# Kernel tuning notes

Hardware: AMD Instinct MI355X
Metric: run time of the kernel (lower is better)

## Reference

```python
import jax, jax.numpy as jnp
import numpy as np

B, P, ENC = 128, 196, 512
H = 512   # must equal ENC (gate * awe elementwise in original)
E = 512   # embed size
A = 512   # attention dim
V = 32000
L = 20    # caption length; decode steps T = L - 1


def setup_inputs() -> dict:
    key = jax.random.key(0)
    ks = jax.random.split(key, 24)
    s = 0.02
    features = jax.random.normal(ks[0], (B, P, ENC), jnp.float32)
    captions = jax.random.randint(ks[1], (B, L), 0, V)
    # lengths sorted descending (pack_padded_sequence contract); force max = L
    len_np = np.sort(np.array(jax.random.randint(ks[2], (B,), 2, L + 1)))[::-1].copy()
    len_np[0] = L
    lengths = jnp.asarray(len_np, jnp.int32)
    rn = lambda k, sh: jax.random.normal(k, sh, jnp.float32) * s
    return {
        "features": features, "captions": captions, "lengths": lengths,
        "w_enc_att": rn(ks[3], (A, ENC)), "b_enc_att": rn(ks[4], (A,)),
        "w_dec_att": rn(ks[5], (A, H)), "b_dec_att": rn(ks[6], (A,)),
        "w_full": rn(ks[7], (A,)), "b_full": rn(ks[8], (1,)),
        "embed_w": rn(ks[9], (V, E)),
        "w_ih": rn(ks[10], (4 * H, E + ENC)), "b_ih": rn(ks[11], (4 * H,)),
        "w_hh": rn(ks[12], (4 * H, H)), "b_hh": rn(ks[13], (4 * H,)),
        "w_init_h": rn(ks[14], (H, ENC)), "b_init_h": rn(ks[15], (H,)),
        "w_init_c": rn(ks[16], (H, ENC)), "b_init_c": rn(ks[17], (H,)),
        "w_beta": rn(ks[18], (H, ENC)), "b_beta": rn(ks[19], (H,)),
        "w_fc": rn(ks[20], (V, H)), "b_fc": rn(ks[21], (V,)),
    }


def _decode(features, captions, lengths, w_enc_att, b_enc_att, w_dec_att,
            b_dec_att, w_full, b_full, embed_w, w_ih, b_ih, w_hh, b_hh,
            w_init_h, b_init_h, w_init_c, b_init_c, w_beta, b_beta, w_fc, b_fc):
    T = captions.shape[1] - 1  # static max decode length
    dec_len = lengths - 1      # [B]
    emb = embed_w[captions]    # [B, L, E]
    fmean = features.mean(axis=1)                       # [B, ENC]
    h0 = fmean @ w_init_h.T + b_init_h                  # [B, H]
    c0 = fmean @ w_init_c.T + b_init_c
    att1 = features @ w_enc_att.T + b_enc_att           # [B, P, A] (precomputed, step-invariant)

    xs_emb = jnp.swapaxes(emb[:, :T, :], 0, 1)          # [T, B, E]
    active = jnp.arange(T)[:, None] < dec_len[None, :]  # [T, B], mimics batch_size_t slicing

    def step(carry, xs):
        h, c = carry
        x_t, act = xs                                   # [B,E], [B]
        m = act[:, None]
        # additive attention
        att2 = h @ w_dec_att.T + b_dec_att              # [B, A]
        e = jnp.einsum('bpa,a->bp', jax.nn.relu(att1 + att2[:, None, :]), w_full) + b_full[0]
        alpha = jax.nn.softmax(e, axis=1)               # [B, P]
        awe = jnp.einsum('bp,bpe->be', alpha, features) # [B, ENC]
        gate = jax.nn.sigmoid(h @ w_beta.T + b_beta)    # [B, H] (H == ENC)
        awe = gate * awe
        # LSTMCell (torch gate order i, f, g, o)
        z = jnp.concatenate([x_t, awe], axis=1)         # [B, E+ENC]
        gates = z @ w_ih.T + b_ih + h @ w_hh.T + b_hh   # [B, 4H]
        i_g, f_g, g_g, o_g = jnp.split(gates, 4, axis=1)
        c_new = jax.nn.sigmoid(f_g) * c + jax.nn.sigmoid(i_g) * jnp.tanh(g_g)
        h_new = jax.nn.sigmoid(o_g) * jnp.tanh(c_new)
        # inactive rows keep old state (torch only updates h[:batch_size_t])
        h2 = jnp.where(m, h_new, h)
        c2 = jnp.where(m, c_new, c)
        preds = h_new @ w_fc.T + b_fc                   # dropout in eval mode (identity)
        preds = jnp.where(m, preds, 0.0)
        alpha_o = jnp.where(m, alpha, 0.0)
        return (h2, c2), (preds, alpha_o)

    (_, _), (preds_t, alphas_t) = jax.lax.scan(step, (h0, c0), (xs_emb, active))
    predictions = jnp.swapaxes(preds_t, 0, 1)           # [B, T, V]
    alphas = jnp.swapaxes(alphas_t, 0, 1)               # [B, T, P]
    return predictions, alphas


def reference(features, captions, lengths, w_enc_att, b_enc_att, w_dec_att,
              b_dec_att, w_full, b_full, embed_w, w_ih, b_ih, w_hh, b_hh,
              w_init_h, b_init_h, w_init_c, b_init_c, w_beta, b_beta, w_fc, b_fc):
    return _decode(features, captions, lengths, w_enc_att, b_enc_att, w_dec_att,
                   b_dec_att, w_full, b_full, embed_w, w_ih, b_ih, w_hh, b_hh,
                   w_init_h, b_init_h, w_init_c, b_init_c, w_beta, b_beta,
                   w_fc, b_fc)
```

## Files before the change

kernel.cpp:

```cpp
#include <hip/hip_runtime.h>
#include <hip/hip_bf16.h>

typedef __attribute__((ext_vector_type(8))) short short8;
typedef __attribute__((ext_vector_type(4))) float floatx4;

#define NB 128
#define NP 196
#define NH 512
#define NV 32000
#define NT 19

__device__ __forceinline__ float bf2f(short s) {
  unsigned int u = ((unsigned int)(unsigned short)s) << 16;
  return __builtin_bit_cast(float, u);
}
__device__ __forceinline__ short f2bf(float f) {
  unsigned int u = __builtin_bit_cast(unsigned int, f);
  unsigned int lsb = (u >> 16) & 1u;
  u += 0x7fffu + lsb;
  return (short)(u >> 16);
}
__device__ __forceinline__ float sigf(float x) { return 1.f / (1.f + expf(-x)); }
__device__ __forceinline__ float ldw(int fl, const void* p, int i) {
  return fl ? bf2f(((const short*)p)[i]) : ((const float*)p)[i];
}

__global__ void k_detect(const unsigned int* __restrict__ w, int* __restrict__ flagp) {
  __shared__ int cnt;
  if (threadIdx.x == 0) cnt = 0;
  __syncthreads();
  int local = 0;
  for (int i = threadIdx.x; i < 4096; i += 256) {
    unsigned int lo = w[i] & 0xFFFFu;
    unsigned int ex = (lo >> 7) & 0xFFu;
    if (ex >= 110u && ex <= 135u) local++;
  }
  atomicAdd(&cnt, local);
  __syncthreads();
  if (threadIdx.x == 0) *flagp = (cnt > 2048) ? 1 : 0;
}

__global__ void k_convall(const void* __restrict__ s0, const void* __restrict__ s1,
                          const void* __restrict__ s2, const void* __restrict__ s3,
                          const void* __restrict__ s4, const void* __restrict__ s5,
                          const void* __restrict__ s6, const void* __restrict__ s7,
                          const void* __restrict__ s8, const void* __restrict__ s9,
                          short* __restrict__ dst, const int* __restrict__ flagp) {
  int fl = *flagp;
  const int totc = 50069504 / 8;
  for (int c = blockIdx.x * 256 + threadIdx.x; c < totc; c += gridDim.x * 256) {
    int i = c * 8;
    const void* src;
    int off;
    if (i < 12845056)      { src = s0; off = i; }
    else if (i < 29229056) { src = s1; off = i - 12845056; }
    else if (i < 45613056) { src = s2; off = i - 29229056; }
    else if (i < 47710208) { src = s3; off = i - 45613056; }
    else if (i < 48758784) { src = s4; off = i - 47710208; }
    else if (i < 49020928) { src = s5; off = i - 48758784; }
    else if (i < 49283072) { src = s6; off = i - 49020928; }
    else if (i < 49545216) { src = s7; off = i - 49283072; }
    else if (i < 49807360) { src = s8; off = i - 49545216; }
    else                   { src = s9; off = i - 49807360; }
    if (fl) {
      ((short8*)dst)[c] = *(const short8*)((const short*)src + off);
    } else {
      const float* sp = (const float*)src + off;
      short8 o;
#pragma unroll
      for (int j = 0; j < 8; ++j) o[j] = f2bf(sp[j]);
      ((short8*)dst)[c] = o;
    }
  }
}

__global__ void k_fmean(const short* __restrict__ feat, short* __restrict__ fmean) {
  int b = blockIdx.x;
  for (int e = threadIdx.x; e < NH; e += 256) {
    float s = 0.f;
    const short* fp = feat + (size_t)b * (NP * NH) + e;
    for (int p = 0; p < NP; ++p) s += bf2f(fp[p * NH]);
    fmean[b * NH + e] = f2bf(s * (1.f / 196.f));
  }
}

__global__ void k_init(const short* __restrict__ fmean,
                       const short* __restrict__ w_init_h, const void* __restrict__ b_init_h,
                       const short* __restrict__ w_init_c, const void* __restrict__ b_init_c,
                       short* __restrict__ hbuf, float* __restrict__ cbuf,
                       const int* __restrict__ flagp) {
  int fl = *flagp;
  int wave = threadIdx.x >> 6, lane = threadIdx.x & 63;
  int rlo = lane & 15, quad = lane >> 4;
  int n = (blockIdx.x * 4 + wave) * 16 + rlo;
  const short* brow = (n < 512 ? w_init_h + (size_t)n * 512 : w_init_c + (size_t)(n - 512) * 512) + quad * 8;
  const short* arow = fmean + rlo * 512 + quad * 8;
  floatx4 acc[8];
#pragma unroll
  for (int mt = 0; mt < 8; ++mt) acc[mt] = (floatx4){0.f, 0.f, 0.f, 0.f};
  for (int k = 0; k < 512; k += 32) {
    short8 bfr = *(const short8*)(brow + k);
#pragma unroll
    for (int mt = 0; mt < 8; ++mt) {
      short8 afr = *(const short8*)(arow + mt * (16 * 512) + k);
      acc[mt] = __builtin_amdgcn_mfma_f32_16x16x32_bf16(afr, bfr, acc[mt], 0, 0, 0);
    }
  }
  float bias = (n < 512) ? ldw(fl, b_init_h, n) : ldw(fl, b_init_c, n - 512);
#pragma unroll
  for (int mt = 0; mt < 8; ++mt)
#pragma unroll
    for (int r = 0; r < 4; ++r) {
      int bb = mt * 16 + quad * 4 + r;
      float v = acc[mt][r] + bias;
      if (n < 512) hbuf[bb * 512 + n] = f2bf(v);
      else cbuf[bb * 512 + (n - 512)] = v;
    }
}

__global__ void k_att1(const short* __restrict__ feat, const short* __restrict__ w_enc,
                       const void* __restrict__ b_enc, short* __restrict__ att1,
                       const int* __restrict__ flagp) {
  int fl = *flagp;
  int wave = threadIdx.x >> 6, lane = threadIdx.x & 63;
  int rlo = lane & 15, quad = lane >> 4;
  int n = (blockIdx.x * 4 + wave) * 16 + rlo;
  int mbase = blockIdx.y * 128;
  const short* brow = w_enc + (size_t)n * 512 + quad * 8;
  const short* arow = feat + (size_t)(mbase + rlo) * 512 + quad * 8;
  floatx4 acc[8];
#pragma unroll
  for (int mt = 0; mt < 8; ++mt) acc[mt] = (floatx4){0.f, 0.f, 0.f, 0.f};
  for (int k = 0; k < 512; k += 32) {
    short8 bfr = *(const short8*)(brow + k);
#pragma unroll
    for (int mt = 0; mt < 8; ++mt) {
      short8 afr = *(const short8*)(arow + (size_t)mt * (16 * 512) + k);
      acc[mt] = __builtin_amdgcn_mfma_f32_16x16x32_bf16(afr, bfr, acc[mt], 0, 0, 0);
    }
  }
  float bias = ldw(fl, b_enc, n);
#pragma unroll
  for (int mt = 0; mt < 8; ++mt)
#pragma unroll
    for (int r = 0; r < 4; ++r) {
      int m = mbase + mt * 16 + quad * 4 + r;
      att1[(size_t)m * 512 + n] = f2bf(acc[mt][r] + bias);
    }
}

__global__ void k_xpart(const int* __restrict__ captions, const short* __restrict__ embed_w,
                        const short* __restrict__ w_ih, const void* __restrict__ b_ih,
                        const void* __restrict__ b_hh, float* __restrict__ xp,
                        const int* __restrict__ flagp) {
  int fl = *flagp;
  int wave = threadIdx.x >> 6, lane = threadIdx.x & 63;
  int rlo = lane & 15, quad = lane >> 4;
  int t = blockIdx.y;
  int n = (blockIdx.x * 4 + wave) * 16 + rlo;
  const short* brow = w_ih + (size_t)n * 1024 + quad * 8;
  int tok[8];
#pragma unroll
  for (int mt = 0; mt < 8; ++mt) tok[mt] = captions[(mt * 16 + rlo) * 20 + t];
  floatx4 acc[8];
#pragma unroll
  for (int mt = 0; mt < 8; ++mt) acc[mt] = (floatx4){0.f, 0.f, 0.f, 0.f};
  for (int k = 0; k < 512; k += 32) {
    short8 bfr = *(const short8*)(brow + k);
#pragma unroll
    for (int mt = 0; mt < 8; ++mt) {
      short8 afr = *(const short8*)(embed_w + (size_t)tok[mt] * 512 + quad * 8 + k);
      acc[mt] = __builtin_amdgcn_mfma_f32_16x16x32_bf16(afr, bfr, acc[mt], 0, 0, 0);
    }
  }
  float bias = ldw(fl, b_ih, n) + ldw(fl, b_hh, n);
#pragma unroll
  for (int mt = 0; mt < 8; ++mt)
#pragma unroll
    for (int r = 0; r < 4; ++r) {
      int bb = mt * 16 + quad * 4 + r;
      xp[((size_t)t * 128 + bb) * 2048 + n] = acc[mt][r] + bias;
    }
}

__global__ void k_hproj(const short* __restrict__ hbuf,
                        const short* __restrict__ w_dec, const void* __restrict__ b_dec,
                        const short* __restrict__ w_beta, const void* __restrict__ b_beta,
                        const short* __restrict__ w_hh, float* __restrict__ abuf,
                        const int* __restrict__ flagp) {
  int fl = *flagp;
  int wave = threadIdx.x >> 6, lane = threadIdx.x & 63;
  int rlo = lane & 15, quad = lane >> 4;
  int n = (blockIdx.x * 4 + wave) * 16 + rlo;
  const short* brow;
  float bias;
  if (n < 512)       { brow = w_dec  + (size_t)n * 512;          bias = ldw(fl, b_dec, n); }
  else if (n < 1024) { brow = w_beta + (size_t)(n - 512) * 512;  bias = ldw(fl, b_beta, n - 512); }
  else               { brow = w_hh   + (size_t)(n - 1024) * 512; bias = 0.f; }
  brow += quad * 8;
  const short* arow = hbuf + rlo * 512 + quad * 8;
  floatx4 acc[8];
#pragma unroll
  for (int mt = 0; mt < 8; ++mt) acc[mt] = (floatx4){0.f, 0.f, 0.f, 0.f};
  for (int k = 0; k < 512; k += 32) {
    short8 bfr = *(const short8*)(brow + k);
#pragma unroll
    for (int mt = 0; mt < 8; ++mt) {
      short8 afr = *(const short8*)(arow + mt * (16 * 512) + k);
      acc[mt] = __builtin_amdgcn_mfma_f32_16x16x32_bf16(afr, bfr, acc[mt], 0, 0, 0);
    }
  }
#pragma unroll
  for (int mt = 0; mt < 8; ++mt)
#pragma unroll
    for (int r = 0; r < 4; ++r) {
      int bb = mt * 16 + quad * 4 + r;
      abuf[(size_t)bb * 3072 + n] = acc[mt][r] + bias;
    }
}

__global__ void k_score(const short* __restrict__ att1, const float* __restrict__ abuf,
                        const void* __restrict__ w_full, float* __restrict__ escore,
                        const int* __restrict__ flagp) {
  int fl = *flagp;
  int wave = threadIdx.x >> 6, lane = threadIdx.x & 63;
  int gw = blockIdx.x * 4 + wave;
  int r0 = gw * 8;
  float wfr[8];
#pragma unroll
  for (int j = 0; j < 8; ++j) wfr[j] = ldw(fl, w_full, lane * 8 + j);
#pragma unroll
  for (int rr = 0; rr < 8; ++rr) {
    int r = r0 + rr;
    int b = r / 196;
    const float* a2 = abuf + (size_t)b * 3072 + lane * 8;
    floatx4 a2a = *(const floatx4*)a2;
    floatx4 a2b = *(const floatx4*)(a2 + 4);
    short8 v = *(const short8*)(att1 + (size_t)r * 512 + lane * 8);
    float s = 0.f;
    s += fmaxf(bf2f(v[0]) + a2a[0], 0.f) * wfr[0];
    s += fmaxf(bf2f(v[1]) + a2a[1], 0.f) * wfr[1];
    s += fmaxf(bf2f(v[2]) + a2a[2], 0.f) * wfr[2];
    s += fmaxf(bf2f(v[3]) + a2a[3], 0.f) * wfr[3];
    s += fmaxf(bf2f(v[4]) + a2b[0], 0.f) * wfr[4];
    s += fmaxf(bf2f(v[5]) + a2b[1], 0.f) * wfr[5];
    s += fmaxf(bf2f(v[6]) + a2b[2], 0.f) * wfr[6];
    s += fmaxf(bf2f(v[7]) + a2b[3], 0.f) * wfr[7];
#pragma unroll
    for (int off = 32; off >= 1; off >>= 1) s += __shfl_xor(s, off, 64);
    if (lane == 0) escore[r] = s;
  }
}

__global__ void k_ctx(const float* __restrict__ escore, const short* __restrict__ feat,
                      const float* __restrict__ abuf, const int* __restrict__ lengths,
                      short* __restrict__ awe, void* __restrict__ d_out,
                      const int* __restrict__ flagp, int t) {
  int fl = *flagp;
  int ec = blockIdx.x;
  int b = blockIdx.y;
  int tid = threadIdx.x, wave = tid >> 6, lane = tid & 63;
  __shared__ float sm[196];
  __shared__ float psum[4][128];
  for (int p = tid; p < NP; p += 256) sm[p] = escore[b * NP + p];
  __syncthreads();
  bool act = t < (lengths[b] - 1);
  if (wave == 0) {
    float v0 = sm[lane], v1 = sm[lane + 64], v2 = sm[lane + 128];
    float v3 = (lane < 4) ? sm[lane + 192] : -1e30f;
    float m = fmaxf(fmaxf(v0, v1), fmaxf(v2, v3));
#pragma unroll
    for (int off = 32; off >= 1; off >>= 1) m = fmaxf(m, __shfl_xor(m, off, 64));
    float e0 = expf(v0 - m), e1 = expf(v1 - m), e2 = expf(v2 - m);
    float e3 = (lane < 4) ? expf(v3 - m) : 0.f;
    float s = e0 + e1 + e2 + e3;
#pragma unroll
    for (int off = 32; off >= 1; off >>= 1) s += __shfl_xor(s, off, 64);
    float inv = 1.f / s;
    float a0 = e0 * inv, a1 = e1 * inv, a2 = e2 * inv, a3 = e3 * inv;
    sm[lane] = a0; sm[lane + 64] = a1; sm[lane + 128] = a2;
    if (lane < 4) sm[lane + 192] = a3;
    if (ec == 0) {
      size_t ob = (size_t)NB * NT * NV + ((size_t)b * NT + t) * NP;
      float o0 = act ? a0 : 0.f, o1 = act ? a1 : 0.f, o2 = act ? a2 : 0.f, o3 = act ? a3 : 0.f;
      if (fl) {
        short* op = (short*)d_out;
        op[ob + lane] = f2bf(o0); op[ob + lane + 64] = f2bf(o1); op[ob + lane + 128] = f2bf(o2);
        if (lane < 4) op[ob + lane + 192] = f2bf(o3);
      } else {
        float* op = (float*)d_out;
        op[ob + lane] = o0; op[ob + lane + 64] = o1; op[ob + lane + 128] = o2;
        if (lane < 4) op[ob + lane + 192] = o3;
      }
    }
  }
  __syncthreads();
  int eoff = ec * 128 + lane * 2;
  const short* fb = feat + (size_t)b * (NP * NH) + eoff;
  float acc0 = 0.f, acc1 = 0.f;
  for (int p = wave; p < NP; p += 4) {
    unsigned int u = *(const unsigned int*)(fb + (size_t)p * NH);
    float al = sm[p];
    acc0 = fmaf(al, __builtin_bit_cast(float, u << 16), acc0);
    acc1 = fmaf(al, __builtin_bit_cast(float, u & 0xFFFF0000u), acc1);
  }
  psum[wave][lane * 2] = acc0;
  psum[wave][lane * 2 + 1] = acc1;
  __syncthreads();
  if (tid < 128) {
    int e = ec * 128 + tid;
    float s = psum[0][tid] + psum[1][tid] + psum[2][tid] + psum[3][tid];
    float gate = sigf(abuf[(size_t)b * 3072 + 512 + e]);
    awe[b * NH + e] = f2bf(gate * s);
  }
}

__global__ void k_gates_lstm(const short* __restrict__ awe_bf, const short* __restrict__ w_ih,
                             const float* __restrict__ xp, const float* __restrict__ abuf,
                             const int* __restrict__ lengths, float* __restrict__ cbuf,
                             short* __restrict__ hbuf, short* __restrict__ hnall, int t) {
  int tid = threadIdx.x, wave = tid >> 6, lane = tid & 63;
  int rlo = lane & 15, quad = lane >> 4;
  int n = wave * 512 + blockIdx.x * 16 + rlo;
  const short* brow = w_ih + (size_t)n * 1024 + 512 + quad * 8;
  const short* arow = awe_bf + rlo * 512 + quad * 8;
  floatx4 acc[8];
#pragma unroll
  for (int mt = 0; mt < 8; ++mt) acc[mt] = (floatx4){0.f, 0.f, 0.f, 0.f};
  for (int k = 0; k < 512; k += 32) {
    short8 bfr = *(const short8*)(brow + k);
#pragma unroll
    for (int mt = 0; mt < 8; ++mt) {
      short8 afr = *(const short8*)(arow + mt * (16 * 512) + k);
      acc[mt] = __builtin_amdgcn_mfma_f32_16x16x32_bf16(afr, bfr, acc[mt], 0, 0, 0);
    }
  }
  __shared__ float gsm[4][128][17];
#pragma unroll
  for (int mt = 0; mt < 8; ++mt)
#pragma unroll
    for (int r = 0; r < 4; ++r) {
      int bb = mt * 16 + quad * 4 + r;
      float v = acc[mt][r] + xp[((size_t)t * 128 + bb) * 2048 + n] + abuf[(size_t)bb * 3072 + 1024 + n];
      gsm[wave][bb][rlo] = v;
    }
  __syncthreads();
  for (int idx = tid; idx < 2048; idx += 256) {
    int bb = idx >> 4, jl = idx & 15;
    int j = blockIdx.x * 16 + jl;
    float ig = gsm[0][bb][jl], fg = gsm[1][bb][jl], gg = gsm[2][bb][jl], og = gsm[3][bb][jl];
    float co = cbuf[bb * 512 + j];
    float cn = sigf(fg) * co + sigf(ig) * tanhf(gg);
    float hn = sigf(og) * tanhf(cn);
    hnall[(size_t)t * (128 * 512) + bb * 512 + j] = f2bf(hn);
    if (t < lengths[bb] - 1) {
      cbuf[bb * 512 + j] = cn;
      hbuf[bb * 512 + j] = f2bf(hn);
    }
  }
}

__global__ void k_preds_all(const short* __restrict__ hnall, const short* __restrict__ w_fc,
                            const void* __restrict__ b_fc, const int* __restrict__ lengths,
                            void* __restrict__ d_out, const int* __restrict__ flagp) {
  int fl = *flagp;
  int tid = threadIdx.x, wave = tid >> 6, lane = tid & 63;
  int rlo = lane & 15, quad = lane >> 4;
  int n0 = blockIdx.x * 128;
  int mh = (wave >> 1) * 64;
  int nh = (wave & 1) * 64;
  __shared__ short Al[128 * 128];
  __shared__ short Bl[128 * 128];

  float bias[4];
#pragma unroll
  for (int nf = 0; nf < 4; ++nf) bias[nf] = ldw(fl, b_fc, n0 + nh + nf * 16 + rlo);

  for (int t = 0; t < NT; ++t) {
    floatx4 acc[4][4];
#pragma unroll
    for (int mt = 0; mt < 4; ++mt)
#pragma unroll
      for (int nf = 0; nf < 4; ++nf) acc[mt][nf] = (floatx4){0.f, 0.f, 0.f, 0.f};

    for (int kc = 0; kc < 4; ++kc) {
#pragma unroll
      for (int j = 0; j < 8; ++j) {
        int idx = j * 256 + tid;
        int row = idx >> 4, c8 = idx & 15;
        int sw = (c8 * 16) ^ ((row & 7) << 4);
        short8 va = *(const short8*)(hnall + ((size_t)t * 128 + row) * 512 + kc * 128 + c8 * 8);
        *(short8*)((char*)Al + row * 256 + sw) = va;
        short8 vb = *(const short8*)(w_fc + (size_t)(n0 + row) * 512 + kc * 128 + c8 * 8);
        *(short8*)((char*)Bl + row * 256 + sw) = vb;
      }
      __syncthreads();
#pragma unroll
      for (int kkl = 0; kkl < 4; ++kkl) {
        int kb = kkl * 64 + quad * 16;
        short8 afr[4], bfr[4];
#pragma unroll
        for (int mt = 0; mt < 4; ++mt) {
          int row = mh + mt * 16 + rlo;
          afr[mt] = *(const short8*)((const char*)Al + row * 256 + (kb ^ ((row & 7) << 4)));
        }
#pragma unroll
        for (int nf = 0; nf < 4; ++nf) {
          int row = nh + nf * 16 + rlo;
          bfr[nf] = *(const short8*)((const char*)Bl + row * 256 + (kb ^ ((row & 7) << 4)));
        }
#pragma unroll
        for (int mt = 0; mt < 4; ++mt)
#pragma unroll
          for (int nf = 0; nf < 4; ++nf)
            acc[mt][nf] = __builtin_amdgcn_mfma_f32_16x16x32_bf16(afr[mt], bfr[nf], acc[mt][nf], 0, 0, 0);
      }
      __syncthreads();
    }
#pragma unroll
    for (int mt = 0; mt < 4; ++mt)
#pragma unroll
      for (int r = 0; r < 4; ++r) {
        int bb = mh + mt * 16 + quad * 4 + r;
        bool act = t < lengths[bb] - 1;
#pragma unroll
        for (int nf = 0; nf < 4; ++nf) {
          int n = n0 + nh + nf * 16 + rlo;
          float v = act ? (acc[mt][nf][r] + bias[nf]) : 0.f;
          size_t oi = ((size_t)bb * NT + t) * NV + n;
          if (fl) ((short*)d_out)[oi] = f2bf(v);
          else ((float*)d_out)[oi] = v;
        }
      }
  }
}

extern "C" void kernel_launch(void* const* d_in, const int* in_sizes, int n_in,
                              void* d_out, int out_size, void* d_ws, size_t ws_size,
                              hipStream_t stream) {
  const void* features = d_in[0];
  const int* captions = (const int*)d_in[1];
  const int* lengths = (const int*)d_in[2];
  const void* w_enc_att = d_in[3];
  const void* b_enc_att = d_in[4];
  const void* w_dec_att = d_in[5];
  const void* b_dec_att = d_in[6];
  const void* w_full = d_in[7];
  const void* embed_w = d_in[9];
  const void* w_ih = d_in[10];
  const void* b_ih = d_in[11];
  const void* w_hh = d_in[12];
  const void* b_hh = d_in[13];
  const void* w_init_h = d_in[14];
  const void* b_init_h = d_in[15];
  const void* w_init_c = d_in[16];
  const void* b_init_c = d_in[17];
  const void* w_beta = d_in[18];
  const void* b_beta = d_in[19];
  const void* w_fc = d_in[20];
  const void* b_fc = d_in[21];

  char* ws = (char*)d_ws;
  int* flagp = (int*)ws; ws += 16;
  short* cfeat = (short*)ws; ws += (size_t)12845056 * 2;
  short* cembed = (short*)ws; ws += (size_t)16384000 * 2;
  short* cwfc = (short*)ws; ws += (size_t)16384000 * 2;
  short* cwih = (short*)ws; ws += (size_t)2097152 * 2;
  short* cwhh = (short*)ws; ws += (size_t)1048576 * 2;
  short* cwenc = (short*)ws; ws += (size_t)262144 * 2;
  short* cwdec = (short*)ws; ws += (size_t)262144 * 2;
  short* cwbeta = (short*)ws; ws += (size_t)262144 * 2;
  short* cwinith = (short*)ws; ws += (size_t)262144 * 2;
  short* cwinitc = (short*)ws; ws += (size_t)262144 * 2;
  short* att1 = (short*)ws; ws += (size_t)25088 * 512 * 2;
  float* xp   = (float*)ws; ws += (size_t)2432 * 2048 * 4;
  float* abuf = (float*)ws; ws += (size_t)128 * 3072 * 4;
  float* escore = (float*)ws; ws += (size_t)25088 * 4;
  short* hbuf = (short*)ws; ws += 128 * 512 * 2;
  short* hnall = (short*)ws; ws += (size_t)NT * 128 * 512 * 2;
  short* awe  = (short*)ws; ws += 128 * 512 * 2;
  short* fmean = (short*)ws; ws += 128 * 512 * 2;
  float* cbuf = (float*)ws; ws += 128 * 512 * 4;

  k_detect<<<1, 256, 0, stream>>>((const unsigned int*)features, flagp);
  k_convall<<<2048, 256, 0, stream>>>(features, embed_w, w_fc, w_ih, w_hh,
                                      w_enc_att, w_dec_att, w_beta, w_init_h, w_init_c,
                                      cfeat, flagp);

  k_fmean<<<128, 256, 0, stream>>>(cfeat, fmean);
  k_att1<<<dim3(8, 196), 256, 0, stream>>>(cfeat, cwenc, b_enc_att, att1, flagp);
  k_xpart<<<dim3(32, NT), 256, 0, stream>>>(captions, cembed, cwih, b_ih, b_hh, xp, flagp);
  k_init<<<16, 256, 0, stream>>>(fmean, cwinith, b_init_h, cwinitc, b_init_c, hbuf, cbuf, flagp);

  for (int t = 0; t < NT; ++t) {
    k_hproj<<<48, 256, 0, stream>>>(hbuf, cwdec, b_dec_att, cwbeta, b_beta, cwhh, abuf, flagp);
    k_score<<<784, 256, 0, stream>>>(att1, abuf, w_full, escore, flagp);
    k_ctx<<<dim3(4, 128), 256, 0, stream>>>(escore, cfeat, abuf, lengths, awe, d_out, flagp, t);
    k_gates_lstm<<<32, 256, 0, stream>>>(awe, cwih, xp, abuf, lengths, cbuf, hbuf, hnall, t);
  }
  k_preds_all<<<250, 256, 0, stream>>>(hnall, cwfc, b_fc, lengths, d_out, flagp);
}
```

Baseline: 2.689 ms.

## Keep w_fc tile resident in LDS across timesteps in output projection

The vocab projection kernel now loads a 64-row slice of w_fc (full K=512) into shared memory once and reuses it for all 19 timesteps. Activations are read straight from global memory, so the per-step LDS staging and barriers are gone. The grid doubles to 500 blocks with launch bounds for two blocks per CU, lengths are cached in registers, and output stores become nontemporal. This cuts repeated weight traffic and synchronisation, at the cost of uncoalesced direct global A-fragment loads and a larger LDS footprint.

```diff
diff --git a/kernel.cpp b/kernel.cpp
--- a/kernel.cpp
+++ b/kernel.cpp
@@ -360,76 +360,74 @@
   }
 }
 
-__global__ void k_preds_all(const short* __restrict__ hnall, const short* __restrict__ w_fc,
-                            const void* __restrict__ b_fc, const int* __restrict__ lengths,
-                            void* __restrict__ d_out, const int* __restrict__ flagp) {
+__global__ void __launch_bounds__(256, 2)
+k_preds_all(const short* __restrict__ hnall, const short* __restrict__ w_fc,
+            const void* __restrict__ b_fc, const int* __restrict__ lengths,
+            void* __restrict__ d_out, const int* __restrict__ flagp) {
   int fl = *flagp;
   int tid = threadIdx.x, wave = tid >> 6, lane = tid & 63;
   int rlo = lane & 15, quad = lane >> 4;
-  int n0 = blockIdx.x * 128;
-  int mh = (wave >> 1) * 64;
-  int nh = (wave & 1) * 64;
-  __shared__ short Al[128 * 128];
-  __shared__ short Bl[128 * 128];
+  int n0 = blockIdx.x * 64;
+  int mw = wave * 32;
+  __shared__ short Bl[64 * 512];
+
+#pragma unroll
+  for (int j = 0; j < 16; ++j) {
+    int idx = j * 256 + tid;
+    int row = idx >> 6, c8 = idx & 63;
+    int sw = (c8 * 16) ^ ((row & 7) << 4);
+    short8 vb = *(const short8*)(w_fc + (size_t)(n0 + row) * 512 + c8 * 8);
+    *(short8*)((char*)Bl + row * 1024 + sw) = vb;
+  }
+  __syncthreads();
 
   float bias[4];
-#pragma unroll
-  for (int nf = 0; nf < 4; ++nf) bias[nf] = ldw(fl, b_fc, n0 + nh + nf * 16 + rlo);
+  int lenr[2][4];
+#pragma unroll
+  for (int nf = 0; nf < 4; ++nf) bias[nf] = ldw(fl, b_fc, n0 + nf * 16 + rlo);
+#pragma unroll
+  for (int mt = 0; mt < 2; ++mt)
+#pragma unroll
+    for (int r = 0; r < 4; ++r) lenr[mt][r] = lengths[mw + mt * 16 + quad * 4 + r];
 
   for (int t = 0; t < NT; ++t) {
-    floatx4 acc[4][4];
-#pragma unroll
-    for (int mt = 0; mt < 4; ++mt)
+    floatx4 acc[2][4];
+#pragma unroll
+    for (int mt = 0; mt < 2; ++mt)
 #pragma unroll
       for (int nf = 0; nf < 4; ++nf) acc[mt][nf] = (floatx4){0.f, 0.f, 0.f, 0.f};
-
-    for (int kc = 0; kc < 4; ++kc) {
-#pragma unroll
-      for (int j = 0; j < 8; ++j) {
-        int idx = j * 256 + tid;
-        int row = idx >> 4, c8 = idx & 15;
-        int sw = (c8 * 16) ^ ((row & 7) << 4);
-        short8 va = *(const short8*)(hnall + ((size_t)t * 128 + row) * 512 + kc * 128 + c8 * 8);
-        *(short8*)((char*)Al + row * 256 + sw) = va;
-        short8 vb = *(const short8*)(w_fc + (size_t)(n0 + row) * 512 + kc * 128 + c8 * 8);
-        *(short8*)((char*)Bl + row * 256 + sw) = vb;
+    const short* abase = hnall + (size_t)t * (128 * 512);
+#pragma unroll
+    for (int ks = 0; ks < 16; ++ks) {
+      short8 afr[2], bfr[4];
+#pragma unroll
+      for (int mt = 0; mt < 2; ++mt)
+        afr[mt] = *(const short8*)(abase + (size_t)(mw + mt * 16 + rlo) * 512 + ks * 32 + quad * 8);
+#pragma unroll
+      for (int nf = 0; nf < 4; ++nf) {
+        int row = nf * 16 + rlo;
+        bfr[nf] = *(const short8*)((const char*)Bl + row * 1024 +
+                                   ((ks * 64 + quad * 16) ^ ((row & 7) << 4)));
       }
-      __syncthreads();
-#pragma unroll
-      for (int kkl = 0; kkl < 4; ++kkl) {
-        int kb = kkl * 64 + quad * 16;
-        short8 afr[4], bfr[4];
-#pragma unroll
-        for (int mt = 0; mt < 4; ++mt) {
-          int row = mh + mt * 16 + rlo;
-          afr[mt] = *(const short8*)((const char*)Al + row * 256 + (kb ^ ((row & 7) << 4)));
-        }
+#pragma unroll
+      for (int mt = 0; mt < 2; ++mt)
+#pragma unroll
+        for (int nf = 0; nf < 4; ++nf)
+          acc[mt][nf] = __builtin_amdgcn_mfma_f32_16x16x32_bf16(afr[mt], bfr[nf], acc[mt][nf], 0, 0, 0);
+    }
+#pragma unroll
+    for (int mt = 0; mt < 2; ++mt)
+#pragma unroll
+      for (int r = 0; r < 4; ++r) {
+        int bb = mw + mt * 16 + quad * 4 + r;
+        bool act = t < lenr[mt][r] - 1;
 #pragma unroll
         for (int nf = 0; nf < 4; ++nf) {
-          int row = nh + nf * 16 + rlo;
-          bfr[nf] = *(const short8*)((const char*)Bl + row * 256 + (kb ^ ((row & 7) << 4)));
-        }
-#pragma unroll
-        for (int mt = 0; mt < 4; ++mt)
-#pragma unroll
-          for (int nf = 0; nf < 4; ++nf)
-            acc[mt][nf] = __builtin_amdgcn_mfma_f32_16x16x32_bf16(afr[mt], bfr[nf], acc[mt][nf], 0, 0, 0);
-      }
-      __syncthreads();
-    }
-#pragma unroll
-    for (int mt = 0; mt < 4; ++mt)
-#pragma unroll
-      for (int r = 0; r < 4; ++r) {
-        int bb = mh + mt * 16 + quad * 4 + r;
-        bool act = t < lengths[bb] - 1;
-#pragma unroll
-        for (int nf = 0; nf < 4; ++nf) {
-          int n = n0 + nh + nf * 16 + rlo;
+          int n = n0 + nf * 16 + rlo;
           float v = act ? (acc[mt][nf][r] + bias[nf]) : 0.f;
           size_t oi = ((size_t)bb * NT + t) * NV + n;
-          if (fl) ((short*)d_out)[oi] = f2bf(v);
-          else ((float*)d_out)[oi] = v;
+          if (fl) __builtin_nontemporal_store(f2bf(v), &((short*)d_out)[oi]);
+          else __builtin_nontemporal_store(v, &((float*)d_out)[oi]);
         }
       }
   }
@@ -498,5 +496,5 @@
     k_ctx<<<dim3(4, 128), 256, 0, stream>>>(escore, cfeat, abuf, lengths, awe, d_out, flagp, t);
     k_gates_lstm<<<32, 256, 0, stream>>>(awe, cwih, xp, abuf, lengths, cbuf, hbuf, hnall, t);
   }
-  k_preds_all<<<250, 256, 0, stream>>>(hnall, cwfc, b_fc, lengths, d_out, flagp);
-}
+  k_preds_all<<<500, 256, 0, stream>>>(hnall, cwfc, b_fc, lengths, d_out, flagp);
+}
```

Result: faster. 2.336 ms (-13.1%).
